# Kernel tuning notes

Measured on AMD Instinct MI355X. Metric: run time of the kernel, lower is better.

The kernel has to match this reference:

```python
import jax, jax.numpy as jnp
import numpy as np

B, T, H, D, O = 64, 4096, 256, 128, 128
EPS = 1e-5


def setup_inputs() -> dict:
    key = jax.random.key(0)
    ks = jax.random.split(key, 20)
    s = lambda *sh: 1.0 / np.sqrt(sh[-1])
    inp = {
        "motion_input": jax.random.normal(ks[0], (B, D), jnp.float32),
        "last_hidden": jax.random.normal(ks[1], (1, B, H), jnp.float32),
        "encoder_outputs": jax.random.normal(ks[2], (T, B, H), jnp.float32),
        # Attn: Linear(2H -> H) and scoring vector v
        "attn_W": jax.random.normal(ks[3], (H, 2 * H), jnp.float32) * s(H, 2 * H),
        "attn_b": jnp.zeros((H,), jnp.float32),
        "v": jax.random.normal(ks[4], (H,), jnp.float32) * (1.0 / np.sqrt(H)),
        # pre_linear: Linear(D+H -> H) + BatchNorm1d(H)
        "pre_W": jax.random.normal(ks[5], (H, D + H), jnp.float32) * s(H, D + H),
        "pre_b": jnp.zeros((H,), jnp.float32),
        "bn_gamma": jnp.ones((H,), jnp.float32),
        "bn_beta": jnp.zeros((H,), jnp.float32),
        # single-layer GRU (PyTorch gate order: r, z, n)
        "W_ih": jax.random.normal(ks[6], (3 * H, H), jnp.float32) * s(3 * H, H),
        "b_ih": jnp.zeros((3 * H,), jnp.float32),
        "W_hh": jax.random.normal(ks[7], (3 * H, H), jnp.float32) * s(3 * H, H),
        "b_hh": jnp.zeros((3 * H,), jnp.float32),
        # output projection
        "out_W": jax.random.normal(ks[8], (O, H), jnp.float32) * s(O, H),
        "out_b": jnp.zeros((O,), jnp.float32),
    }
    return inp


def reference(motion_input, last_hidden, encoder_outputs, attn_W, attn_b, v,
              pre_W, pre_b, bn_gamma, bn_beta, W_ih, b_ih, W_hh, b_hh,
              out_W, out_b):
    h_prev = last_hidden[-1]                      # [B,H]
    # --- Bahdanau additive attention ---
    # attn_W acts on cat([hidden_rep, enc], -1); split into hidden/enc parts
    W_h, W_e = attn_W[:, :H], attn_W[:, H:]       # each [H,H]
    hid_proj = h_prev @ W_h.T + attn_b            # [B,H]
    enc_proj = jnp.einsum('tbh,gh->btg', encoder_outputs, W_e)  # [B,T,H]
    energy = jnp.tanh(hid_proj[:, None, :] + enc_proj)          # [B,T,H]
    scores = jnp.einsum('bth,h->bt', energy, v)   # [B,T]
    attn_weights = jax.nn.softmax(scores, axis=1) # [B,T]
    context = jnp.einsum('bt,tbh->bh', attn_weights, encoder_outputs)  # [B,H]
    # --- pre_linear: Linear + BatchNorm1d (training stats) + ReLU ---
    x = jnp.concatenate([motion_input, context], axis=-1)  # [B,D+H]
    x = x @ pre_W.T + pre_b                                 # [B,H]
    mu = jnp.mean(x, axis=0)
    var = jnp.var(x, axis=0)
    x = (x - mu) * jax.lax.rsqrt(var + EPS) * bn_gamma + bn_beta
    x = jax.nn.relu(x)
    # --- single-step GRU cell (PyTorch formulation, gates r,z,n) ---
    gi = x @ W_ih.T + b_ih                         # [B,3H]
    gh = h_prev @ W_hh.T + b_hh                    # [B,3H]
    i_r, i_z, i_n = gi[:, :H], gi[:, H:2*H], gi[:, 2*H:]
    h_r, h_z, h_n = gh[:, :H], gh[:, H:2*H], gh[:, 2*H:]
    r = jax.nn.sigmoid(i_r + h_r)
    z = jax.nn.sigmoid(i_z + h_z)
    n = jnp.tanh(i_n + r * h_n)
    h_new = (1.0 - z) * n + z * h_prev             # [B,H]
    # --- output projection ---
    output = h_new @ out_W.T + out_b               # [B,O]
    hidden = h_new[None, :, :]                     # [1,B,H]
    return output, hidden, attn_weights[:, None, :]  # attn in shape [B,1,T]
```

## Files before the change

### kernel.cpp

```cpp
#include <hip/hip_runtime.h>
#include <math.h>

#define B 64
#define T 4096
#define H 256
#define D 128
#define O 128
#define EPS 1e-5f

#define TCHUNK 16
#define CHUNKS 8

typedef _Float16 half8 __attribute__((ext_vector_type(8)));
typedef float f32x4 __attribute__((ext_vector_type(4)));

__device__ __forceinline__ float tanh_fast(float x) {
  return 1.f - 2.f / (__expf(2.f * x) + 1.f);
}

__global__ __launch_bounds__(256) void k0_permW(const float* __restrict__ attn_W,
                                               _Float16* __restrict__ Bperm) {
  int idx = blockIdx.x * 256 + threadIdx.x;
  int j = idx & 7;
  int l = (idx >> 3) & 63;
  int kt = (idx >> 9) & 7;
  int nt = idx >> 12;
  int g = nt * 16 + (l & 15);
  int k = kt * 32 + ((l >> 4) << 3) + j;
  Bperm[idx] = (_Float16)attn_W[(size_t)g * (2 * H) + H + k];
}

__global__ __launch_bounds__(256) void k1_hidproj_gh(
    const float* __restrict__ last_hidden, const float* __restrict__ attn_W,
    const float* __restrict__ attn_b, const float* __restrict__ W_hh,
    const float* __restrict__ b_hh, float* __restrict__ hid_proj,
    float* __restrict__ gh) {
  int b = blockIdx.x;
  int g = threadIdx.x;
  __shared__ __align__(16) float hp[H];
  hp[g] = last_hidden[b * H + g];
  __syncthreads();
  const float4* hp4 = reinterpret_cast<const float4*>(hp);
  const float4* wr = reinterpret_cast<const float4*>(attn_W + (size_t)g * (2 * H));
  float acc = attn_b[g];
#pragma unroll 8
  for (int h4 = 0; h4 < H / 4; ++h4) {
    float4 w = wr[h4], x = hp4[h4];
    acc += w.x * x.x + w.y * x.y + w.z * x.z + w.w * x.w;
  }
  hid_proj[b * H + g] = acc;
#pragma unroll
  for (int k = 0; k < 3; ++k) {
    int row = k * H + g;
    const float4* whr = reinterpret_cast<const float4*>(W_hh + (size_t)row * H);
    float a2 = b_hh[row];
#pragma unroll 8
    for (int h4 = 0; h4 < H / 4; ++h4) {
      float4 w = whr[h4], x = hp4[h4];
      a2 += w.x * x.x + w.y * x.y + w.z * x.z + w.w * x.w;
    }
    gh[(size_t)b * (3 * H) + row] = a2;
  }
}

__global__ __launch_bounds__(512, 3) void k2_scores_wreg(
    const float* __restrict__ enc, const _Float16* __restrict__ Bperm,
    const float* __restrict__ hid_proj, const float* __restrict__ v,
    float* __restrict__ scores) {
  const int b = blockIdx.y;
  const int tid = threadIdx.x;
  const int wave = tid >> 6;
  const int lane = tid & 63;
  const int r = lane & 15;
  const int grp = lane >> 4;

  __shared__ __align__(16) _Float16 Alds[2][4 * 8 * 64 * 8];
  __shared__ float spart[8][64];

  const half8* bp = reinterpret_cast<const half8*>(Bperm);
  const int ntb = wave * 2;
  half8 wfrag[2][8];
#pragma unroll
  for (int n = 0; n < 2; ++n)
#pragma unroll
    for (int kt = 0; kt < 8; ++kt)
      wfrag[n][kt] = bp[((ntb + n) * 8 + kt) * 64 + lane];

  float hpv[2][4], vg[2][4];
#pragma unroll
  for (int n = 0; n < 2; ++n)
#pragma unroll
    for (int i = 0; i < 4; ++i) {
      int g = (ntb + n) * 16 + grp * 4 + i;
      hpv[n][i] = hid_proj[b * H + g];
      vg[n][i] = v[g];
    }

  const int rbase = tid & 7;
  const int kg = (tid >> 3) & 31;
  const int ihi = (tid >> 8) & 1;
  const int kt_s = kg >> 2;
  const int lhi = (kg & 3) << 4;
  const int cbase = blockIdx.x * CHUNKS;

  float4 x0[4], x1[4];
  auto stage_load = [&](int c) {
    const int t0 = (cbase + c) * 64;
#pragma unroll
    for (int i = 0; i < 4; ++i) {
      int row = i * 16 + ihi * 8 + rbase;
      const float* src = enc + ((size_t)(t0 + row) * B + b) * H + kg * 8;
      x0[i] = *reinterpret_cast<const float4*>(src);
      x1[i] = *reinterpret_cast<const float4*>(src + 4);
    }
  };
  auto stage_write = [&](int buf) {
#pragma unroll
    for (int i = 0; i < 4; ++i) {
      int row = i * 16 + ihi * 8 + rbase;
      half8 hh;
      hh[0] = (_Float16)x0[i].x; hh[1] = (_Float16)x0[i].y;
      hh[2] = (_Float16)x0[i].z; hh[3] = (_Float16)x0[i].w;
      hh[4] = (_Float16)x1[i].x; hh[5] = (_Float16)x1[i].y;
      hh[6] = (_Float16)x1[i].z; hh[7] = (_Float16)x1[i].w;
      int m = row >> 4;
      int lane_s = lhi | (row & 15);
      *reinterpret_cast<half8*>(
          &Alds[buf][(((m * 8) + kt_s) * 64 + lane_s) * 8]) = hh;
    }
  };

  stage_load(0);
  stage_write(0);
  __syncthreads();

  for (int c = 0; c < CHUNKS; ++c) {
    const int buf = c & 1;

    f32x4 acc[2][4];
#pragma unroll
    for (int n = 0; n < 2; ++n)
#pragma unroll
      for (int m = 0; m < 4; ++m) acc[n][m] = (f32x4){0.f, 0.f, 0.f, 0.f};

#pragma unroll
    for (int kt = 0; kt < 8; ++kt) {
#pragma unroll
      for (int m = 0; m < 4; ++m) {
        half8 e = *reinterpret_cast<const half8*>(
            &Alds[buf][((m * 8 + kt) * 64 + lane) * 8]);
        acc[0][m] = __builtin_amdgcn_mfma_f32_16x16x32_f16(
            wfrag[0][kt], e, acc[0][m], 0, 0, 0);
        acc[1][m] = __builtin_amdgcn_mfma_f32_16x16x32_f16(
            wfrag[1][kt], e, acc[1][m], 0, 0, 0);
      }
    }

    if (c + 1 < CHUNKS) stage_load(c + 1);

#pragma unroll
    for (int m = 0; m < 4; ++m) {
      float s = 0.f;
#pragma unroll
      for (int n = 0; n < 2; ++n)
#pragma unroll
        for (int i = 0; i < 4; ++i)
          s += vg[n][i] * tanh_fast(acc[n][m][i] + hpv[n][i]);
      s += __shfl_xor(s, 16);
      s += __shfl_xor(s, 32);
      if (grp == 0) spart[wave][m * 16 + r] = s;
    }
    __syncthreads();
    if (tid < 64) {
      float sv = 0.f;
#pragma unroll
      for (int w = 0; w < 8; ++w) sv += spart[w][tid];
      scores[(size_t)b * T + (cbase + c) * 64 + tid] = sv;
    }
    if (c + 1 < CHUNKS) stage_write(buf ^ 1);
    __syncthreads();
  }
}

__global__ __launch_bounds__(256) void k3_softmax(
    const float* __restrict__ scores, float* __restrict__ attn_out) {
  int b = blockIdx.x;
  int tid = threadIdx.x;
  float vals[16];
  const float4* sp = reinterpret_cast<const float4*>(scores + (size_t)b * T);
#pragma unroll
  for (int i = 0; i < 4; ++i) {
    float4 x = sp[i * 256 + tid];
    vals[i * 4 + 0] = x.x; vals[i * 4 + 1] = x.y;
    vals[i * 4 + 2] = x.z; vals[i * 4 + 3] = x.w;
  }
  float m = -INFINITY;
#pragma unroll
  for (int i = 0; i < 16; ++i) m = fmaxf(m, vals[i]);
  for (int off = 32; off > 0; off >>= 1) m = fmaxf(m, __shfl_xor(m, off));
  __shared__ float redm[4];
  int wave = tid >> 6, lane = tid & 63;
  if (lane == 0) redm[wave] = m;
  __syncthreads();
  m = fmaxf(fmaxf(redm[0], redm[1]), fmaxf(redm[2], redm[3]));
  float s = 0.f;
#pragma unroll
  for (int i = 0; i < 16; ++i) {
    vals[i] = expf(vals[i] - m);
    s += vals[i];
  }
  for (int off = 32; off > 0; off >>= 1) s += __shfl_xor(s, off);
  __shared__ float reds[4];
  if (lane == 0) reds[wave] = s;
  __syncthreads();
  s = reds[0] + reds[1] + reds[2] + reds[3];
  float inv = 1.f / s;
  float4* op = reinterpret_cast<float4*>(attn_out + (size_t)b * T);
#pragma unroll
  for (int i = 0; i < 4; ++i) {
    float4 x;
    x.x = vals[i * 4 + 0] * inv; x.y = vals[i * 4 + 1] * inv;
    x.z = vals[i * 4 + 2] * inv; x.w = vals[i * 4 + 3] * inv;
    op[i * 256 + tid] = x;
  }
}

__global__ __launch_bounds__(256) void k4_ctx_part(
    const float* __restrict__ enc, const float* __restrict__ attn_w,
    float* __restrict__ ctx_part) {
  int chunk = blockIdx.x;
  int b = blockIdx.y;
  int tid = threadIdx.x;
  int h4 = tid & 63;
  int tsub = tid >> 6;
  int tstart = chunk * (T / TCHUNK);
  float4 acc = {0.f, 0.f, 0.f, 0.f};
  const float* wrow = attn_w + (size_t)b * T;
#pragma unroll 8
  for (int t = tstart + tsub; t < tstart + T / TCHUNK; t += 4) {
    float w = wrow[t];
    float4 e = *reinterpret_cast<const float4*>(
        enc + ((size_t)t * B + b) * H + h4 * 4);
    acc.x += w * e.x; acc.y += w * e.y; acc.z += w * e.z; acc.w += w * e.w;
  }
  __shared__ float4 red[4][64];
  red[tsub][h4] = acc;
  __syncthreads();
  if (tid < 64) {
    float4 a = red[0][tid], b2 = red[1][tid], c = red[2][tid], d2 = red[3][tid];
    float4 r;
    r.x = a.x + b2.x + c.x + d2.x;
    r.y = a.y + b2.y + c.y + d2.y;
    r.z = a.z + b2.z + c.z + d2.z;
    r.w = a.w + b2.w + c.w + d2.w;
    *reinterpret_cast<float4*>(ctx_part + ((size_t)chunk * B + b) * H + tid * 4) = r;
  }
}

__global__ __launch_bounds__(256) void k5_prelinear(
    const float* __restrict__ ctx_part, const float* __restrict__ motion,
    const float* __restrict__ pre_W, const float* __restrict__ pre_b,
    float* __restrict__ xpre) {
  int b = blockIdx.x;
  int g = threadIdx.x;
  __shared__ __align__(16) float cm[D + H];
  float c = 0.f;
#pragma unroll
  for (int p = 0; p < TCHUNK; ++p) c += ctx_part[((size_t)p * B + b) * H + g];
  cm[D + g] = c;
  if (g < D) cm[g] = motion[b * D + g];
  __syncthreads();
  const float4* cm4 = reinterpret_cast<const float4*>(cm);
  const float4* wr = reinterpret_cast<const float4*>(pre_W + (size_t)g * (D + H));
  float acc = pre_b[g];
#pragma unroll 8
  for (int j = 0; j < (D + H) / 4; ++j) {
    float4 w = wr[j], x = cm4[j];
    acc += w.x * x.x + w.y * x.y + w.z * x.z + w.w * x.w;
  }
  xpre[b * H + g] = acc;
}

__global__ __launch_bounds__(256) void k5b_bn(
    const float* __restrict__ xpre, const float* __restrict__ gamma,
    const float* __restrict__ beta, float* __restrict__ xn) {
  int g = threadIdx.x;
  float mu = 0.f;
  for (int b = 0; b < B; ++b) mu += xpre[b * H + g];
  mu *= (1.f / B);
  float var = 0.f;
  for (int b = 0; b < B; ++b) {
    float d = xpre[b * H + g] - mu;
    var += d * d;
  }
  var *= (1.f / B);
  float sc = gamma[g] * rsqrtf(var + EPS);
  float bi = beta[g];
  for (int b = 0; b < B; ++b) {
    float y = (xpre[b * H + g] - mu) * sc + bi;
    xn[b * H + g] = fmaxf(y, 0.f);
  }
}

__global__ __launch_bounds__(256) void k6_gru_out(
    const float* __restrict__ xn, const float* __restrict__ gh,
    const float* __restrict__ W_ih, const float* __restrict__ b_ih,
    const float* __restrict__ last_hidden, const float* __restrict__ out_W,
    const float* __restrict__ out_b, float* __restrict__ out_output,
    float* __restrict__ out_hidden) {
  int b = blockIdx.x;
  int g = threadIdx.x;
  __shared__ __align__(16) float xr[H];
  __shared__ __align__(16) float hn[H];
  xr[g] = xn[b * H + g];
  __syncthreads();
  const float4* xr4 = reinterpret_cast<const float4*>(xr);
  float gi[3];
#pragma unroll
  for (int k = 0; k < 3; ++k) {
    int row = k * H + g;
    const float4* wr = reinterpret_cast<const float4*>(W_ih + (size_t)row * H);
    float a = b_ih[row];
#pragma unroll 8
    for (int h4 = 0; h4 < H / 4; ++h4) {
      float4 w = wr[h4], x = xr4[h4];
      a += w.x * x.x + w.y * x.y + w.z * x.z + w.w * x.w;
    }
    gi[k] = a;
  }
  float hr = gh[(size_t)b * 3 * H + g];
  float hz = gh[(size_t)b * 3 * H + H + g];
  float hnn = gh[(size_t)b * 3 * H + 2 * H + g];
  float r = 1.f / (1.f + expf(-(gi[0] + hr)));
  float z = 1.f / (1.f + expf(-(gi[1] + hz)));
  float n = tanhf(gi[2] + r * hnn);
  float hprev = last_hidden[b * H + g];
  float hnew = (1.f - z) * n + z * hprev;
  out_hidden[b * H + g] = hnew;
  hn[g] = hnew;
  __syncthreads();
  if (g < O) {
    const float4* hn4 = reinterpret_cast<const float4*>(hn);
    const float4* wr = reinterpret_cast<const float4*>(out_W + (size_t)g * H);
    float a = out_b[g];
#pragma unroll 8
    for (int h4 = 0; h4 < H / 4; ++h4) {
      float4 w = wr[h4], x = hn4[h4];
      a += w.x * x.x + w.y * x.y + w.z * x.z + w.w * x.w;
    }
    out_output[b * O + g] = a;
  }
}

extern "C" void kernel_launch(void* const* d_in, const int* in_sizes, int n_in,
                              void* d_out, int out_size, void* d_ws,
                              size_t ws_size, hipStream_t stream) {
  (void)in_sizes; (void)n_in; (void)out_size; (void)ws_size;
  const float* motion      = (const float*)d_in[0];
  const float* last_hidden = (const float*)d_in[1];
  const float* enc         = (const float*)d_in[2];
  const float* attn_W      = (const float*)d_in[3];
  const float* attn_b      = (const float*)d_in[4];
  const float* v           = (const float*)d_in[5];
  const float* pre_W       = (const float*)d_in[6];
  const float* pre_b       = (const float*)d_in[7];
  const float* bn_g        = (const float*)d_in[8];
  const float* bn_b        = (const float*)d_in[9];
  const float* W_ih        = (const float*)d_in[10];
  const float* b_ih        = (const float*)d_in[11];
  const float* W_hh        = (const float*)d_in[12];
  const float* b_hh        = (const float*)d_in[13];
  const float* out_W       = (const float*)d_in[14];
  const float* out_b       = (const float*)d_in[15];

  float* out = (float*)d_out;
  float* out_output = out;
  float* out_hidden = out + B * O;
  float* out_attn   = out + B * O + B * H;

  float* ws = (float*)d_ws;
  float* sc = ws;
  float* cp = sc + (size_t)B * T;
  float* hp = cp + (size_t)TCHUNK * B * H;
  float* gh = hp + (size_t)B * H;
  float* xp = gh + (size_t)3 * B * H;
  float* xn = xp + (size_t)B * H;
  _Float16* Bperm = (_Float16*)(xn + (size_t)B * H);

  k0_permW<<<256, 256, 0, stream>>>(attn_W, Bperm);
  k1_hidproj_gh<<<B, 256, 0, stream>>>(last_hidden, attn_W, attn_b, W_hh, b_hh,
                                       hp, gh);
  k2_scores_wreg<<<dim3(T / (64 * CHUNKS), B), 512, 0, stream>>>(enc, Bperm,
                                                                 hp, v, sc);
  k3_softmax<<<B, 256, 0, stream>>>(sc, out_attn);
  k4_ctx_part<<<dim3(TCHUNK, B), 256, 0, stream>>>(enc, out_attn, cp);
  k5_prelinear<<<B, 256, 0, stream>>>(cp, motion, pre_W, pre_b, xp);
  k5b_bn<<<1, 256, 0, stream>>>(xp, bn_g, bn_b, xn);
  k6_gru_out<<<B, 256, 0, stream>>>(xn, gh, W_ih, b_ih, last_hidden, out_W,
                                    out_b, out_output, out_hidden);
}
```

Before: 206.8 us.

## Drop per-chunk LDS score reduction, write per-wave partials, fuse into softmax

The score kernel no longer reduces the 8 per-wave partial scores through shared memory with an extra barrier. Each wave writes its partial to a global [B,T,8] buffer, and the softmax kernel sums the 8 partials as it loads them. The global load for the next chunk is issued before the MFMA loop and the LDS write is moved before the tanh epilogue, leaving one barrier per chunk. The tanh uses a prescaled hidden projection and a hardware reciprocal, and the occupancy hint drops from 3 to 2. This trades more global traffic for the score partials (8x larger workspace) and higher register pressure from the earlier prefetch for fewer barriers and better overlap.

Measured after the change: 221.6 us. 1.07x slower.

```diff
diff --git a/kernel.cpp b/kernel.cpp
--- a/kernel.cpp
+++ b/kernel.cpp
@@ -14,8 +14,10 @@
 typedef _Float16 half8 __attribute__((ext_vector_type(8)));
 typedef float f32x4 __attribute__((ext_vector_type(4)));
 
-__device__ __forceinline__ float tanh_fast(float x) {
-  return 1.f - 2.f / (__expf(2.f * x) + 1.f);
+__device__ __forceinline__ float rcp_fast(float x) {
+  float r;
+  asm("v_rcp_f32 %0, %1" : "=v"(r) : "v"(x));
+  return r;
 }
 
 __global__ __launch_bounds__(256) void k0_permW(const float* __restrict__ attn_W,
@@ -63,10 +65,10 @@
   }
 }
 
-__global__ __launch_bounds__(512, 3) void k2_scores_wreg(
+__global__ __launch_bounds__(512, 2) void k2_scores_lean(
     const float* __restrict__ enc, const _Float16* __restrict__ Bperm,
     const float* __restrict__ hid_proj, const float* __restrict__ v,
-    float* __restrict__ scores) {
+    float* __restrict__ scpart) {
   const int b = blockIdx.y;
   const int tid = threadIdx.x;
   const int wave = tid >> 6;
@@ -75,7 +77,6 @@
   const int grp = lane >> 4;
 
   __shared__ __align__(16) _Float16 Alds[2][4 * 8 * 64 * 8];
-  __shared__ float spart[8][64];
 
   const half8* bp = reinterpret_cast<const half8*>(Bperm);
   const int ntb = wave * 2;
@@ -86,13 +87,13 @@
     for (int kt = 0; kt < 8; ++kt)
       wfrag[n][kt] = bp[((ntb + n) * 8 + kt) * 64 + lane];
 
-  float hpv[2][4], vg[2][4];
+  float hpv2[2][4], vg[2][4];
 #pragma unroll
   for (int n = 0; n < 2; ++n)
 #pragma unroll
     for (int i = 0; i < 4; ++i) {
       int g = (ntb + n) * 16 + grp * 4 + i;
-      hpv[n][i] = hid_proj[b * H + g];
+      hpv2[n][i] = 2.f * hid_proj[b * H + g];
       vg[n][i] = v[g];
     }
 
@@ -136,6 +137,7 @@
 
   for (int c = 0; c < CHUNKS; ++c) {
     const int buf = c & 1;
+    if (c + 1 < CHUNKS) stage_load(c + 1);
 
     f32x4 acc[2][4];
 #pragma unroll
@@ -156,7 +158,7 @@
       }
     }
 
-    if (c + 1 < CHUNKS) stage_load(c + 1);
+    if (c + 1 < CHUNKS) stage_write(buf ^ 1);
 
 #pragma unroll
     for (int m = 0; m < 4; ++m) {
@@ -164,35 +166,33 @@
 #pragma unroll
       for (int n = 0; n < 2; ++n)
 #pragma unroll
-        for (int i = 0; i < 4; ++i)
-          s += vg[n][i] * tanh_fast(acc[n][m][i] + hpv[n][i]);
+        for (int i = 0; i < 4; ++i) {
+          float e2 = __expf(fmaf(2.f, acc[n][m][i], hpv2[n][i]));
+          float t = fmaf(-2.f, rcp_fast(e2 + 1.f), 1.f);
+          s = fmaf(vg[n][i], t, s);
+        }
       s += __shfl_xor(s, 16);
       s += __shfl_xor(s, 32);
-      if (grp == 0) spart[wave][m * 16 + r] = s;
+      if (grp == 0) {
+        size_t t = (size_t)b * T + (cbase + c) * 64 + m * 16 + r;
+        scpart[t * 8 + wave] = s;
+      }
     }
     __syncthreads();
-    if (tid < 64) {
-      float sv = 0.f;
-#pragma unroll
-      for (int w = 0; w < 8; ++w) sv += spart[w][tid];
-      scores[(size_t)b * T + (cbase + c) * 64 + tid] = sv;
-    }
-    if (c + 1 < CHUNKS) stage_write(buf ^ 1);
-    __syncthreads();
   }
 }
 
 __global__ __launch_bounds__(256) void k3_softmax(
-    const float* __restrict__ scores, float* __restrict__ attn_out) {
+    const float* __restrict__ scpart, float* __restrict__ attn_out) {
   int b = blockIdx.x;
   int tid = threadIdx.x;
   float vals[16];
-  const float4* sp = reinterpret_cast<const float4*>(scores + (size_t)b * T);
-#pragma unroll
-  for (int i = 0; i < 4; ++i) {
-    float4 x = sp[i * 256 + tid];
-    vals[i * 4 + 0] = x.x; vals[i * 4 + 1] = x.y;
-    vals[i * 4 + 2] = x.z; vals[i * 4 + 3] = x.w;
+#pragma unroll
+  for (int i = 0; i < 16; ++i) {
+    const float4* pp = reinterpret_cast<const float4*>(
+        scpart + ((size_t)b * T + tid * 16 + i) * 8);
+    float4 a = pp[0], c = pp[1];
+    vals[i] = a.x + a.y + a.z + a.w + c.x + c.y + c.z + c.w;
   }
   float m = -INFINITY;
 #pragma unroll
@@ -215,13 +215,13 @@
   __syncthreads();
   s = reds[0] + reds[1] + reds[2] + reds[3];
   float inv = 1.f / s;
-  float4* op = reinterpret_cast<float4*>(attn_out + (size_t)b * T);
+  float4* op = reinterpret_cast<float4*>(attn_out + (size_t)b * T + tid * 16);
 #pragma unroll
   for (int i = 0; i < 4; ++i) {
     float4 x;
     x.x = vals[i * 4 + 0] * inv; x.y = vals[i * 4 + 1] * inv;
     x.z = vals[i * 4 + 2] * inv; x.w = vals[i * 4 + 3] * inv;
-    op[i * 256 + tid] = x;
+    op[i] = x;
   }
 }
 
@@ -379,20 +379,20 @@
   float* out_attn   = out + B * O + B * H;
 
   float* ws = (float*)d_ws;
-  float* sc = ws;
-  float* cp = sc + (size_t)B * T;
-  float* hp = cp + (size_t)TCHUNK * B * H;
-  float* gh = hp + (size_t)B * H;
-  float* xp = gh + (size_t)3 * B * H;
-  float* xn = xp + (size_t)B * H;
+  float* scpart = ws;
+  float* cp   = scpart + (size_t)8 * B * T;
+  float* hp   = cp + (size_t)TCHUNK * B * H;
+  float* gh   = hp + (size_t)B * H;
+  float* xp   = gh + (size_t)3 * B * H;
+  float* xn   = xp + (size_t)B * H;
   _Float16* Bperm = (_Float16*)(xn + (size_t)B * H);
 
   k0_permW<<<256, 256, 0, stream>>>(attn_W, Bperm);
   k1_hidproj_gh<<<B, 256, 0, stream>>>(last_hidden, attn_W, attn_b, W_hh, b_hh,
                                        hp, gh);
-  k2_scores_wreg<<<dim3(T / (64 * CHUNKS), B), 512, 0, stream>>>(enc, Bperm,
-                                                                 hp, v, sc);
-  k3_softmax<<<B, 256, 0, stream>>>(sc, out_attn);
+  k2_scores_lean<<<dim3(T / (64 * CHUNKS), B), 512, 0, stream>>>(enc, Bperm,
+                                                                 hp, v, scpart);
+  k3_softmax<<<B, 256, 0, stream>>>(scpart, out_attn);
   k4_ctx_part<<<dim3(TCHUNK, B), 256, 0, stream>>>(enc, out_attn, cp);
   k5_prelinear<<<B, 256, 0, stream>>>(cp, motion, pre_W, pre_b, xp);
   k5b_bn<<<1, 256, 0, stream>>>(xp, bn_g, bn_b, xn);
```
